# Optimization experiments

Measured on AMD Instinct MI355X. Metric: run time of the kernel, lower is better.

The kernel has to match this reference:

```python
import jax, jax.numpy as jnp
import numpy as np


def setup_inputs() -> dict:
    key = jax.random.key(0)
    k1, k2 = jax.random.split(key)
    x = jax.random.normal(k1, (64, 32, 32, 128), dtype=jnp.float32)
    embeddings = jax.random.normal(k2, (128, 1024), dtype=jnp.float32)  # (embedding_dim, num_embeddings)
    return {"x": x, "embeddings": embeddings}


def reference(x, embeddings):
    d = embeddings.shape[0]
    flat = x.reshape(-1, d)  # [N, d]
    # squared L2 distances: ||f||^2 + ||e||^2 - 2 f.e
    similarity = flat @ embeddings  # [N, K]
    distances = (jnp.sum(flat * flat, axis=1, keepdims=True)
                 + jnp.sum(embeddings * embeddings, axis=0)
                 - 2.0 * similarity)
    idx = jnp.argmin(distances, axis=1)  # [N]
    # gather codes (equivalent to one_hot @ embeddings^T)
    quantized = embeddings.T[idx].reshape(x.shape)
    # straight-through estimator
    quantized = x + jax.lax.stop_gradient(quantized - x)
    return quantized
```

## Files before the change

kernel.cpp:

```cpp
#include <hip/hip_runtime.h>


#define NROWS 65536
#define DDIM 128
#define KCODES 1024
#define MARGIN1 0.30f

typedef __attribute__((ext_vector_type(8))) short short8;
typedef __attribute__((ext_vector_type(16))) float f32x16;

__device__ inline ushort f2bf(float f) {
    union { float f; unsigned u; } v; v.f = f;
    unsigned r = v.u + 0x7fffu + ((v.u >> 16) & 1u);
    return (ushort)(r >> 16);
}
__device__ inline float bf2f(ushort b) {
    union { unsigned u; float f; } v; v.u = ((unsigned)b) << 16;
    return v.f;
}

__device__ inline void gload_lds16(const uint4* g, uint4* lds) {
    __builtin_amdgcn_global_load_lds((const __attribute__((address_space(1))) void*)g,
                                     (__attribute__((address_space(3))) void*)lds,
                                     16, 0, 0);
}

__global__ void k_prep(const float* __restrict__ x, const float* __restrict__ e,
                       float* __restrict__ et, float* __restrict__ nrm,
                       double* __restrict__ nrm64, uint4* __restrict__ epq,
                       unsigned* __restrict__ nhl, uint4* __restrict__ xp,
                       int* __restrict__ wlc) {
    const int gid = blockIdx.x * blockDim.x + threadIdx.x;

    if (gid == 0) { wlc[0] = 0; wlc[1] = 0; }

    {
        int lane = gid & 63, c = (gid >> 6) & 7, rt = gid >> 9;
        int row = rt * 32 + (lane & 31);
        int kbase = c * 16 + ((lane >> 5) << 3);
        const float4* xr4 = reinterpret_cast<const float4*>(x + (size_t)row * DDIM + kbase);
        float4 u = xr4[0], v = xr4[1];
        float fv[8] = {u.x, u.y, u.z, u.w, v.x, v.y, v.z, v.w};
        union { ushort s[8]; uint4 q; } pk;
        #pragma unroll
        for (int j = 0; j < 8; ++j) pk.s[j] = f2bf(fv[j]);
        xp[gid] = pk.q;
    }

    if (gid < 131072) {
        int d = gid >> 10, k = gid & 1023;
        et[k * DDIM + d] = e[gid];
    }

    if (gid < 16384) {
        int lane = gid & 63, c = (gid >> 6) & 7, nt = gid >> 9;
        int col = nt * 32 + (lane & 31);
        int kbase = c * 16 + ((lane >> 5) << 3);
        union { ushort s[8]; uint4 q; } pk;
        #pragma unroll
        for (int j = 0; j < 8; ++j)
            pk.s[j] = f2bf(e[(kbase + j) * KCODES + col]);
        epq[(size_t)nt * 512 + c * 64 + lane] = pk.q;
    }

    if (gid >= 32768 && gid < 32768 + 8192) {
        int t2 = gid - 32768;
        int k = t2 >> 3, part = t2 & 7;
        double s = 0.0;
        #pragma unroll
        for (int j = 0; j < 16; ++j) {
            double v = (double)e[(part * 16 + j) * KCODES + k];
            s = fma(v, v, s);
        }
        #pragma unroll
        for (int m = 1; m < 8; m <<= 1) s += __shfl_xor(s, m);
        if (part == 0) {
            nrm64[k] = s; nrm[k] = (float)s;
            float t0 = (float)(-0.5 * s);
            ushort hb = f2bf(t0);
            ushort lb = f2bf(t0 - bf2f(hb));
            nhl[k] = (unsigned)hb | ((unsigned)lb << 16);
        }
    }
}

__global__ __launch_bounds__(256, 2) void k_argmin32(const uint4* __restrict__ xp,
                                                     const uint4* __restrict__ epq,
                                                     const unsigned* __restrict__ nhl,
                                                     unsigned* __restrict__ pb1,
                                                     float* __restrict__ pb2) {
    __shared__ uint4 sbuf[4096];
    __shared__ unsigned snhl[256];

    const int tid = threadIdx.x;
    const int lane = tid & 63;
    const int w = tid >> 6;
    const int kq = blockIdx.x & 3;
    const int rg = blockIdx.x >> 2;
    const int rtA = rg * 8 + w * 2;
    const int rtB = rtA + 1;
    const int lrow = lane & 31;
    const int lgrp = lane >> 5;

    #pragma unroll
    for (int i = 0; i < 16; ++i)
        gload_lds16(epq + (size_t)kq * 4096 + i * 256 + tid,
                    &sbuf[i * 256 + (w << 6)]);
    if (tid < 64)
        gload_lds16(reinterpret_cast<const uint4*>(nhl) + kq * 64 + tid,
                    reinterpret_cast<uint4*>(snhl));

    short8 ahA[8], ahB[8];
    #pragma unroll
    for (int c = 0; c < 8; ++c) {
        union { uint4 q; short8 s; } ua, ub;
        ua.q = xp[(size_t)rtA * 512 + c * 64 + lane];
        ub.q = xp[(size_t)rtB * 512 + c * 64 + lane];
        ahA[c] = ua.s; ahB[c] = ub.s;
    }
    short8 bx = {0, 0, 0, 0, 0, 0, 0, 0};
    if (lgrp == 0) { bx[0] = (short)0x3F80; bx[1] = (short)0x3F80; }
    const unsigned cid4 = (unsigned)(lgrp << 2);

    asm volatile("s_waitcnt vmcnt(0)" ::: "memory");
    __syncthreads();

    float kA1 = -3.4e38f, kA2 = -3.4e38f;
    float kB1 = -3.4e38f, kB2 = -3.4e38f;

    for (int t = 0; t < 8; ++t) {
        f32x16 aA, aB;
        #pragma unroll
        for (int r = 0; r < 16; ++r) { aA[r] = 0.f; aB[r] = 0.f; }

        #pragma unroll
        for (int c = 0; c < 8; ++c) {
            union { uint4 q; short8 s; } ef;
            ef.q = sbuf[t * 512 + c * 64 + lane];
            aA = __builtin_amdgcn_mfma_f32_32x32x16_bf16(ef.s, ahA[c], aA, 0, 0, 0);
            aB = __builtin_amdgcn_mfma_f32_32x32x16_bf16(ef.s, ahB[c], aB, 0, 0, 0);
        }
        unsigned hl = snhl[t * 32 + lrow];
        short8 ax = {0, 0, 0, 0, 0, 0, 0, 0};
        if (lgrp == 0) { ax[0] = (short)(hl & 0xFFFF); ax[1] = (short)(hl >> 16); }
        aA = __builtin_amdgcn_mfma_f32_32x32x16_bf16(ax, bx, aA, 0, 0, 0);
        aB = __builtin_amdgcn_mfma_f32_32x32x16_bf16(ax, bx, aB, 0, 0, 0);

        #pragma unroll
        for (int r = 0; r < 16; ++r) {
            unsigned cid = (unsigned)((t << 5) | ((r & 3) + ((r >> 2) << 3))) | cid4;
            float keyA = __uint_as_float((__float_as_uint(aA[r]) & 0xFFFFFF00u) | cid);
            float keyB = __uint_as_float((__float_as_uint(aB[r]) & 0xFFFFFF00u) | cid);
            kA2 = __builtin_amdgcn_fmed3f(kA1, kA2, keyA);
            kA1 = fmaxf(kA1, keyA);
            kB2 = __builtin_amdgcn_fmed3f(kB1, kB2, keyB);
            kB1 = fmaxf(kB1, keyB);
        }
    }

    {
        float o1 = __shfl_xor(kA1, 32);
        float o2 = __shfl_xor(kA2, 32);
        float m2 = __builtin_amdgcn_fmed3f(kA1, o1, fmaxf(kA2, o2));
        float m1 = fmaxf(kA1, o1);
        if (lane < 32) {
            size_t o = (size_t)kq * NROWS + rtA * 32 + lrow;
            pb1[o] = __float_as_uint(m1);
            pb2[o] = m2;
        }
    }
    {
        float o1 = __shfl_xor(kB1, 32);
        float o2 = __shfl_xor(kB2, 32);
        float m2 = __builtin_amdgcn_fmed3f(kB1, o1, fmaxf(kB2, o2));
        float m1 = fmaxf(kB1, o1);
        if (lane < 32) {
            size_t o = (size_t)kq * NROWS + rtB * 32 + lrow;
            pb1[o] = __float_as_uint(m1);
            pb2[o] = m2;
        }
    }
}

__global__ void k_merge(const unsigned* __restrict__ pb1, const float* __restrict__ pb2,
                        int* __restrict__ idx, int* __restrict__ wlc,
                        int* __restrict__ wl) {
    int r = blockIdx.x * blockDim.x + threadIdx.x;
    float best = -3.4e38f, sec = -3.4e38f;
    unsigned ub = 0; int bq = 0;
    #pragma unroll
    for (int q = 0; q < 4; ++q) {
        unsigned k1 = pb1[(size_t)q * NROWS + r];
        float    s2 = __uint_as_float(__float_as_uint(pb2[(size_t)q * NROWS + r]) & 0xFFFFFF00u);
        float    m  = __uint_as_float(k1 & 0xFFFFFF00u);
        bool t = m > best;
        sec = fmaxf(sec, fmaxf(s2, t ? best : m));
        ub = t ? k1 : ub;
        bq = t ? q : bq;
        best = t ? m : best;
    }
    int code = bq * 256 + (int)(ub & 255u);
    idx[r] = code;
    if (2.f * (best - sec) < MARGIN1) {
        int slot = atomicAdd(wlc, 1);
        wl[slot] = r;
    }
}

__global__ __launch_bounds__(256) void k_rescan(const float* __restrict__ x,
                                                const float* __restrict__ e,
                                                const double* __restrict__ nrm64,
                                                const int* __restrict__ wlc,
                                                const int* __restrict__ wl,
                                                int* __restrict__ idx) {
    __shared__ float  xs[4][DDIM];
    __shared__ double rb1[4][256];
    __shared__ int    ri[4][256];
    const int tid = threadIdx.x, lane = tid & 63, wv = tid >> 6;
    const int n = *wlc;

    for (int i0 = blockIdx.x * 4; i0 < n; i0 += gridDim.x * 4) {
        if (tid < 128) {
            int j = tid >> 5, d4 = tid & 31;
            int ii = i0 + j;
            int row = wl[ii < n ? ii : i0];
            *reinterpret_cast<float4*>(&xs[j][d4 * 4]) =
                *reinterpret_cast<const float4*>(&x[(size_t)row * DDIM + d4 * 4]);
        }
        __syncthreads();

        double acc[4][4];
        #pragma unroll
        for (int kk = 0; kk < 4; ++kk)
            #pragma unroll
            for (int j = 0; j < 4; ++j) acc[kk][j] = 0.0;

        for (int d = 0; d < DDIM; d += 2) {
            double xv0[4], xv1[4];
            #pragma unroll
            for (int j = 0; j < 4; ++j) {
                xv0[j] = (double)xs[j][d];
                xv1[j] = (double)xs[j][d + 1];
            }
            #pragma unroll
            for (int kk = 0; kk < 4; ++kk) {
                double ev0 = (double)e[d * KCODES + kk * 256 + tid];
                double ev1 = (double)e[(d + 1) * KCODES + kk * 256 + tid];
                #pragma unroll
                for (int j = 0; j < 4; ++j) {
                    acc[kk][j] = fma(ev0, xv0[j], acc[kk][j]);
                    acc[kk][j] = fma(ev1, xv1[j], acc[kk][j]);
                }
            }
        }

        #pragma unroll
        for (int j = 0; j < 4; ++j) {
            double b1 = 1e300; int bi = 0;
            #pragma unroll
            for (int kk = 0; kk < 4; ++kk) {
                int k = kk * 256 + tid;
                double s = nrm64[k] - 2.0 * acc[kk][j];
                if (s < b1) { b1 = s; bi = k; }
            }
            rb1[j][tid] = b1; ri[j][tid] = bi;
        }
        __syncthreads();

        {
            double b1 = 1e300; int bi = 0x7FFFFFFF;
            #pragma unroll
            for (int p = 0; p < 4; ++p) {
                int t2 = lane + p * 64;
                double o1 = rb1[wv][t2]; int oi = ri[wv][t2];
                bool take = (o1 < b1) || (o1 == b1 && oi < bi);
                b1 = take ? o1 : b1;
                bi = take ? oi : bi;
            }
            #pragma unroll
            for (int m = 1; m < 64; m <<= 1) {
                double o1 = __shfl_xor(b1, m);
                int    oi = __shfl_xor(bi, m);
                bool take = (o1 < b1) || (o1 == b1 && oi < bi);
                b1 = take ? o1 : b1;
                bi = take ? oi : bi;
            }
            if (lane == 0 && i0 + wv < n)
                idx[wl[i0 + wv]] = bi;
        }
        __syncthreads();
    }
}

__global__ void k_gather(const float* __restrict__ x, const float* __restrict__ et,
                         const int* __restrict__ idxp, float* __restrict__ out) {
    int gid = blockIdx.x * blockDim.x + threadIdx.x;
    int row = gid >> 5, d4 = gid & 31;
    float4 q = reinterpret_cast<const float4*>(et)[(size_t)idxp[row] * 32 + d4];
    float4 xv = reinterpret_cast<const float4*>(x)[gid];
    float4 o;
    o.x = xv.x + (q.x - xv.x);
    o.y = xv.y + (q.y - xv.y);
    o.z = xv.z + (q.z - xv.z);
    o.w = xv.w + (q.w - xv.w);
    reinterpret_cast<float4*>(out)[gid] = o;
}

extern "C" void kernel_launch(void* const* d_in, const int* in_sizes, int n_in,
                              void* d_out, int out_size, void* d_ws, size_t ws_size,
                              hipStream_t stream) {
    const float* x = (const float*)d_in[0];
    const float* e = (const float*)d_in[1];
    float* out = (float*)d_out;

    double*   nrm64 = (double*)d_ws;
    float*    et    = (float*)d_ws + 2048;
    float*    nrm   = et + 131072;
    int*      idx   = (int*)(nrm + 1024);
    int*      wlc   = idx + NROWS;
    int*      wl    = wlc + 4;
    uint4*    epq   = (uint4*)(wl + NROWS);
    unsigned* nhl   = (unsigned*)(epq + 16384);
    unsigned* pb1   = nhl + 1024;
    float*    pb2   = (float*)(pb1 + 4 * NROWS);
    uint4*    xp    = (uint4*)d_out;

    k_prep<<<4096, 256, 0, stream>>>(x, e, et, nrm, nrm64, epq, nhl, xp, wlc);
    k_argmin32<<<1024, 256, 0, stream>>>(xp, epq, nhl, pb1, pb2);
    k_merge<<<NROWS / 256, 256, 0, stream>>>(pb1, pb2, idx, wlc, wl);
    k_rescan<<<1024, 256, 0, stream>>>(x, e, nrm64, wlc, wl, idx);
    k_gather<<<(NROWS * 32) / 256, 256, 0, stream>>>(x, et, idx, out);
}
```

Before: 94.15 us.

## Fuse merge and gather into one kernel, let rescan overwrite output rows

The partial-result merge and the codebook gather/straight-through output now run in a single kernel. Codes are held in shared memory instead of a global idx array, which removes one launch and the idx round trip. The rescan kernel now writes corrected output rows directly for ambiguous rows, overwriting the tentative rows k_finish already wrote. This relies on stream ordering, and those rows are written twice.

```diff
diff --git a/kernel.cpp b/kernel.cpp
--- a/kernel.cpp
+++ b/kernel.cpp
@@ -182,10 +182,18 @@
     }
 }
 
-__global__ void k_merge(const unsigned* __restrict__ pb1, const float* __restrict__ pb2,
-                        int* __restrict__ idx, int* __restrict__ wlc,
-                        int* __restrict__ wl) {
-    int r = blockIdx.x * blockDim.x + threadIdx.x;
+__global__ __launch_bounds__(256) void k_finish(const float* __restrict__ x,
+                                                const float* __restrict__ et,
+                                                const unsigned* __restrict__ pb1,
+                                                const float* __restrict__ pb2,
+                                                int* __restrict__ wlc,
+                                                int* __restrict__ wl,
+                                                float* __restrict__ out) {
+    __shared__ int scode[256];
+    const int tid = threadIdx.x;
+    const int base = blockIdx.x * 256;
+    const int r = base + tid;
+
     float best = -3.4e38f, sec = -3.4e38f;
     unsigned ub = 0; int bq = 0;
     #pragma unroll
@@ -199,20 +207,39 @@
         bq = t ? q : bq;
         best = t ? m : best;
     }
-    int code = bq * 256 + (int)(ub & 255u);
-    idx[r] = code;
+    scode[tid] = bq * 256 + (int)(ub & 255u);
     if (2.f * (best - sec) < MARGIN1) {
         int slot = atomicAdd(wlc, 1);
         wl[slot] = r;
     }
+    __syncthreads();
+
+    const float4* x4  = reinterpret_cast<const float4*>(x);
+    const float4* et4 = reinterpret_cast<const float4*>(et);
+    float4* o4 = reinterpret_cast<float4*>(out);
+    #pragma unroll
+    for (int i = 0; i < 32; ++i) {
+        int j = i * 256 + tid;
+        int rl = j >> 5, d4 = j & 31;
+        size_t g = (size_t)(base + rl) * 32 + d4;
+        float4 q = et4[(size_t)scode[rl] * 32 + d4];
+        float4 xv = x4[g];
+        float4 o;
+        o.x = xv.x + (q.x - xv.x);
+        o.y = xv.y + (q.y - xv.y);
+        o.z = xv.z + (q.z - xv.z);
+        o.w = xv.w + (q.w - xv.w);
+        o4[g] = o;
+    }
 }
 
 __global__ __launch_bounds__(256) void k_rescan(const float* __restrict__ x,
                                                 const float* __restrict__ e,
+                                                const float* __restrict__ et,
                                                 const double* __restrict__ nrm64,
                                                 const int* __restrict__ wlc,
                                                 const int* __restrict__ wl,
-                                                int* __restrict__ idx) {
+                                                float* __restrict__ out) {
     __shared__ float  xs[4][DDIM];
     __shared__ double rb1[4][256];
     __shared__ int    ri[4][256];
@@ -285,25 +312,20 @@
                 b1 = take ? o1 : b1;
                 bi = take ? oi : bi;
             }
-            if (lane == 0 && i0 + wv < n)
-                idx[wl[i0 + wv]] = bi;
+            if (i0 + wv < n && lane < 32) {
+                int row = wl[i0 + wv];
+                float4 q = reinterpret_cast<const float4*>(et)[(size_t)bi * 32 + lane];
+                float4 xv = *reinterpret_cast<const float4*>(&xs[wv][lane * 4]);
+                float4 o;
+                o.x = xv.x + (q.x - xv.x);
+                o.y = xv.y + (q.y - xv.y);
+                o.z = xv.z + (q.z - xv.z);
+                o.w = xv.w + (q.w - xv.w);
+                reinterpret_cast<float4*>(out)[(size_t)row * 32 + lane] = o;
+            }
         }
         __syncthreads();
     }
-}
-
-__global__ void k_gather(const float* __restrict__ x, const float* __restrict__ et,
-                         const int* __restrict__ idxp, float* __restrict__ out) {
-    int gid = blockIdx.x * blockDim.x + threadIdx.x;
-    int row = gid >> 5, d4 = gid & 31;
-    float4 q = reinterpret_cast<const float4*>(et)[(size_t)idxp[row] * 32 + d4];
-    float4 xv = reinterpret_cast<const float4*>(x)[gid];
-    float4 o;
-    o.x = xv.x + (q.x - xv.x);
-    o.y = xv.y + (q.y - xv.y);
-    o.z = xv.z + (q.z - xv.z);
-    o.w = xv.w + (q.w - xv.w);
-    reinterpret_cast<float4*>(out)[gid] = o;
 }
 
 extern "C" void kernel_launch(void* const* d_in, const int* in_sizes, int n_in,
@@ -316,8 +338,7 @@
     double*   nrm64 = (double*)d_ws;
     float*    et    = (float*)d_ws + 2048;
     float*    nrm   = et + 131072;
-    int*      idx   = (int*)(nrm + 1024);
-    int*      wlc   = idx + NROWS;
+    int*      wlc   = (int*)(nrm + 1024);
     int*      wl    = wlc + 4;
     uint4*    epq   = (uint4*)(wl + NROWS);
     unsigned* nhl   = (unsigned*)(epq + 16384);
@@ -327,7 +348,6 @@
 
     k_prep<<<4096, 256, 0, stream>>>(x, e, et, nrm, nrm64, epq, nhl, xp, wlc);
     k_argmin32<<<1024, 256, 0, stream>>>(xp, epq, nhl, pb1, pb2);
-    k_merge<<<NROWS / 256, 256, 0, stream>>>(pb1, pb2, idx, wlc, wl);
-    k_rescan<<<1024, 256, 0, stream>>>(x, e, nrm64, wlc, wl, idx);
-    k_gather<<<(NROWS * 32) / 256, 256, 0, stream>>>(x, et, idx, out);
-}
+    k_finish<<<NROWS / 256, 256, 0, stream>>>(x, et, pb1, pb2, wlc, wl, out);
+    k_rescan<<<1024, 256, 0, stream>>>(x, e, et, nrm64, wlc, wl, out);
+}
```

Result: faster. 91.65 us (median of 2 runs) (-2.7%).
